# Performance work log

Measured on AMD Instinct MI355X. Metric: run time of the kernel, lower is better.

## Reference

```python
import itertools
import jax, jax.numpy as jnp
import numpy as np

GRID = 16384      # self.shape = (GRID,)
LAYERS = 8        # num_layers
SPAN = 2          # span = (2,)
K = 2 * SPAN + 1  # kernel size = 5 (ninputs)
NPOS = 2 ** K     # 32 possible boolean input combos
BATCH = 32
M = 4096          # x width; GRID % M == 0
STRIDE = GRID // M

# bitmask: all 2^K boolean input combinations, shape (NPOS, K)
_BITMASK = jnp.asarray(list(itertools.product(range(2), repeat=K)), dtype=jnp.float32)


def setup_inputs() -> dict:
    key = jax.random.key(0)
    k1, k2 = jax.random.split(key)
    x = jax.random.uniform(k1, (BATCH, M), dtype=jnp.float32)
    toggle_gates = jax.random.uniform(k2, (LAYERS, NPOS, GRID), dtype=jnp.float32)
    return {"x": x, "toggle_gates": toggle_gates}


def _convolve(state):
    # torch convolve(): offsets 0..K-1 via wrap-around roll, then spatial roll by
    # -SPAN to center the window -> neighbor n+i-SPAN (mod GRID) at kernel idx i.
    # jnp.roll(state, SPAN - i) gives out[:, n] = state[:, n + i - SPAN mod GRID].
    return jnp.stack([jnp.roll(state, SPAN - i, axis=1) for i in range(K)], axis=-1)  # (B, N, K)


def reference(x, toggle_gates):
    tw = jax.nn.sigmoid(toggle_gates)  # (L, NPOS, N)
    # embed(): scatter x evenly into the grid, rest is scratch (zeros)
    state = jnp.zeros((x.shape[0], GRID), dtype=x.dtype).at[:, ::STRIDE].set(x)

    def step(s, tw_layer):
        conv = _convolve(s)  # (B, N, K)
        # weight[c, b, n] = prod_i (1 - |bitmask[c, i] - conv[b, n, i]|)
        w = jnp.prod(1.0 - jnp.abs(_BITMASK[:, None, None, :] - conv[None]), axis=-1)  # (C, B, N)
        new = jnp.clip(jnp.einsum('cbn,cn->bn', w, tw_layer), 0.0, 1.0)
        return new, None

    state, _ = jax.lax.scan(step, state, tw)
    # forward returns state[slices] = state[:, ::STRIDE]
    return state[:, ::STRIDE]
```

## Files before the change

kernel.cpp:

```cpp
#include <hip/hip_runtime.h>

#define GRID_N 16384
#define NLAYERS 8
#define NPOS 32
#define BATCH 32
#define MW 4096
#define TILE 64
#define HALO 16
#define WBUF (TILE + 2 * HALO)

__global__ __launch_bounds__(256) void ASIC_44186623541335_kernel(
    const float* __restrict__ x,
    const float* __restrict__ tg,
    float* __restrict__ out)
{
    __shared__ float st[BATCH][WBUF];

    const int tid = threadIdx.x;
    const int tx  = tid & 63;
    const int ty  = tid >> 6;
    const int start = blockIdx.x * TILE;

    for (int f = tid; f < BATCH * WBUF; f += 256) {
        const int b = f / WBUF;
        const int j = f - b * WBUF;
        const int g = (start - HALO + j) & (GRID_N - 1);
        float v = 0.0f;
        if ((g & 3) == 0) v = x[b * MW + (g >> 2)];
        st[b][j] = v;
    }
    __syncthreads();

    float newv[2][8];

    for (int l = 0; l < NLAYERS; ++l) {
        const int h     = 2 * (NLAYERS - 1 - l);
        const int ncols = TILE + 2 * h;
        const int jbase = HALO - h;
        const float* twl = tg + (size_t)l * NPOS * GRID_N;

        #pragma unroll
        for (int p = 0; p < 2; ++p) {
            const int ci = tx + p * 64;
            if (ci < ncols) {
                const int j = jbase + ci;
                const int g = (start - h + ci) & (GRID_N - 1);

                float tw[32];
                #pragma unroll
                for (int c = 0; c < 32; ++c) {
                    const float v = twl[c * GRID_N + g];
                    tw[c] = __builtin_amdgcn_rcpf(1.0f + __expf(-v));
                }

                #pragma unroll
                for (int bb = 0; bb < 8; ++bb) {
                    const int b = ty * 8 + bb;
                    const float s0 = st[b][j - 2];
                    const float s1 = st[b][j - 1];
                    const float s2 = st[b][j];
                    const float s3 = st[b][j + 1];
                    const float s4 = st[b][j + 2];

                    float u[16];
                    #pragma unroll
                    for (int r = 0; r < 16; ++r)
                        u[r] = fmaf(s0, tw[16 + r] - tw[r], tw[r]);
                    #pragma unroll
                    for (int r = 0; r < 8; ++r)
                        u[r] = fmaf(s1, u[8 + r] - u[r], u[r]);
                    #pragma unroll
                    for (int r = 0; r < 4; ++r)
                        u[r] = fmaf(s2, u[4 + r] - u[r], u[r]);
                    #pragma unroll
                    for (int r = 0; r < 2; ++r)
                        u[r] = fmaf(s3, u[2 + r] - u[r], u[r]);
                    float res = fmaf(s4, u[1] - u[0], u[0]);
                    res = fminf(fmaxf(res, 0.0f), 1.0f);
                    newv[p][bb] = res;
                }
            }
        }
        __syncthreads();
        #pragma unroll
        for (int p = 0; p < 2; ++p) {
            const int ci = tx + p * 64;
            if (ci < ncols) {
                const int j = jbase + ci;
                #pragma unroll
                for (int bb = 0; bb < 8; ++bb)
                    st[ty * 8 + bb][j] = newv[p][bb];
            }
        }
        __syncthreads();
    }

    {
        const int g = start + tx;
        if ((g & 3) == 0) {
            const int m = g >> 2;
            #pragma unroll
            for (int bb = 0; bb < 8; ++bb) {
                const int b = ty * 8 + bb;
                out[b * MW + m] = st[b][HALO + tx];
            }
        }
    }
}

extern "C" void kernel_launch(void* const* d_in, const int* in_sizes, int n_in,
                              void* d_out, int out_size, void* d_ws, size_t ws_size,
                              hipStream_t stream) {
    const float* x  = (const float*)d_in[0];
    const float* tg = (const float*)d_in[1];
    float* out = (float*)d_out;
    ASIC_44186623541335_kernel<<<GRID_N / TILE, 256, 0, stream>>>(x, tg, out);
}
```

Before: 93.57 us.

## Halve tile, stage sigmoid gate weights in shared memory with layer-ahead prefetch

Shrinks the spatial tile from 64 to 32 columns, so the grid doubles to 512 blocks and each thread now covers one column instead of up to two. Gate weights for each layer are loaded cooperatively and coalesced, sigmoid is computed once per column into a padded shared-memory table, and the next layer's gates are prefetched into registers while the current layer computes. This replaces per-thread strided global loads and repeated sigmoid evaluation. The cost is more redundant halo work relative to the smaller tile, because the halo stays at 16 columns per side, plus extra shared memory.

```diff
diff --git a/kernel.cpp b/kernel.cpp
--- a/kernel.cpp
+++ b/kernel.cpp
@@ -5,9 +5,10 @@
 #define NPOS 32
 #define BATCH 32
 #define MW 4096
-#define TILE 64
+#define TILE 32
 #define HALO 16
-#define WBUF (TILE + 2 * HALO)
+#define WBUF 64
+#define TWPAD 33
 
 __global__ __launch_bounds__(256) void ASIC_44186623541335_kernel(
     const float* __restrict__ x,
@@ -15,95 +16,110 @@
     float* __restrict__ out)
 {
     __shared__ float st[BATCH][WBUF];
+    __shared__ float twl[WBUF][TWPAD];
 
     const int tid = threadIdx.x;
     const int tx  = tid & 63;
     const int ty  = tid >> 6;
     const int start = blockIdx.x * TILE;
+    const int gcol  = (start - HALO + tx) & (GRID_N - 1);
+
+    float pf[8];
+
+    #pragma unroll
+    for (int k = 0; k < 8; ++k) {
+        const int c = ty + 4 * k;
+        pf[k] = tg[(size_t)c * GRID_N + gcol];
+    }
 
     for (int f = tid; f < BATCH * WBUF; f += 256) {
-        const int b = f / WBUF;
-        const int j = f - b * WBUF;
+        const int b = f >> 6;
+        const int j = f & 63;
         const int g = (start - HALO + j) & (GRID_N - 1);
-        float v = 0.0f;
-        if ((g & 3) == 0) v = x[b * MW + (g >> 2)];
-        st[b][j] = v;
+        st[b][j] = ((g & 3) == 0) ? x[b * MW + (g >> 2)] : 0.0f;
+    }
+
+    #pragma unroll
+    for (int k = 0; k < 8; ++k) {
+        const int c = ty + 4 * k;
+        twl[tx][c] = __builtin_amdgcn_rcpf(1.0f + __expf(-pf[k]));
+    }
+    #pragma unroll
+    for (int k = 0; k < 8; ++k) {
+        const int c = ty + 4 * k;
+        pf[k] = tg[(size_t)NPOS * GRID_N + (size_t)c * GRID_N + gcol];
     }
     __syncthreads();
 
-    float newv[2][8];
-
+    float newv[8];
     for (int l = 0; l < NLAYERS; ++l) {
         const int h     = 2 * (NLAYERS - 1 - l);
         const int ncols = TILE + 2 * h;
-        const int jbase = HALO - h;
-        const float* twl = tg + (size_t)l * NPOS * GRID_N;
+        const int j     = (HALO - h) + tx;
+        const bool act  = tx < ncols;
 
-        #pragma unroll
-        for (int p = 0; p < 2; ++p) {
-            const int ci = tx + p * 64;
-            if (ci < ncols) {
-                const int j = jbase + ci;
-                const int g = (start - h + ci) & (GRID_N - 1);
+        if (act) {
+            float tw[32];
+            #pragma unroll
+            for (int c = 0; c < 32; ++c) tw[c] = twl[j][c];
 
-                float tw[32];
+            #pragma unroll
+            for (int bb = 0; bb < 8; ++bb) {
+                const int b = ty * 8 + bb;
+                const float s0 = st[b][j - 2];
+                const float s1 = st[b][j - 1];
+                const float s2 = st[b][j];
+                const float s3 = st[b][j + 1];
+                const float s4 = st[b][j + 2];
+
+                float u[16];
                 #pragma unroll
-                for (int c = 0; c < 32; ++c) {
-                    const float v = twl[c * GRID_N + g];
-                    tw[c] = __builtin_amdgcn_rcpf(1.0f + __expf(-v));
-                }
-
+                for (int r = 0; r < 16; ++r)
+                    u[r] = fmaf(s0, tw[16 + r] - tw[r], tw[r]);
                 #pragma unroll
-                for (int bb = 0; bb < 8; ++bb) {
-                    const int b = ty * 8 + bb;
-                    const float s0 = st[b][j - 2];
-                    const float s1 = st[b][j - 1];
-                    const float s2 = st[b][j];
-                    const float s3 = st[b][j + 1];
-                    const float s4 = st[b][j + 2];
-
-                    float u[16];
-                    #pragma unroll
-                    for (int r = 0; r < 16; ++r)
-                        u[r] = fmaf(s0, tw[16 + r] - tw[r], tw[r]);
-                    #pragma unroll
-                    for (int r = 0; r < 8; ++r)
-                        u[r] = fmaf(s1, u[8 + r] - u[r], u[r]);
-                    #pragma unroll
-                    for (int r = 0; r < 4; ++r)
-                        u[r] = fmaf(s2, u[4 + r] - u[r], u[r]);
-                    #pragma unroll
-                    for (int r = 0; r < 2; ++r)
-                        u[r] = fmaf(s3, u[2 + r] - u[r], u[r]);
-                    float res = fmaf(s4, u[1] - u[0], u[0]);
-                    res = fminf(fmaxf(res, 0.0f), 1.0f);
-                    newv[p][bb] = res;
-                }
+                for (int r = 0; r < 8; ++r)
+                    u[r] = fmaf(s1, u[8 + r] - u[r], u[r]);
+                #pragma unroll
+                for (int r = 0; r < 4; ++r)
+                    u[r] = fmaf(s2, u[4 + r] - u[r], u[r]);
+                #pragma unroll
+                for (int r = 0; r < 2; ++r)
+                    u[r] = fmaf(s3, u[2 + r] - u[r], u[r]);
+                float res = fmaf(s4, u[1] - u[0], u[0]);
+                newv[bb] = fminf(fmaxf(res, 0.0f), 1.0f);
             }
         }
         __syncthreads();
-        #pragma unroll
-        for (int p = 0; p < 2; ++p) {
-            const int ci = tx + p * 64;
-            if (ci < ncols) {
-                const int j = jbase + ci;
+
+        if (act) {
+            #pragma unroll
+            for (int bb = 0; bb < 8; ++bb)
+                st[ty * 8 + bb][j] = newv[bb];
+        }
+        if (l < NLAYERS - 1) {
+            #pragma unroll
+            for (int k = 0; k < 8; ++k) {
+                const int c = ty + 4 * k;
+                twl[tx][c] = __builtin_amdgcn_rcpf(1.0f + __expf(-pf[k]));
+            }
+            if (l + 2 < NLAYERS) {
+                const float* tn = tg + (size_t)(l + 2) * NPOS * GRID_N;
                 #pragma unroll
-                for (int bb = 0; bb < 8; ++bb)
-                    st[ty * 8 + bb][j] = newv[p][bb];
+                for (int k = 0; k < 8; ++k) {
+                    const int c = ty + 4 * k;
+                    pf[k] = tn[(size_t)c * GRID_N + gcol];
+                }
             }
         }
         __syncthreads();
     }
 
-    {
-        const int g = start + tx;
-        if ((g & 3) == 0) {
-            const int m = g >> 2;
-            #pragma unroll
-            for (int bb = 0; bb < 8; ++bb) {
-                const int b = ty * 8 + bb;
-                out[b * MW + m] = st[b][HALO + tx];
-            }
+    if (tx < TILE && (tx & 3) == 0) {
+        const int m = (start + tx) >> 2;
+        #pragma unroll
+        for (int bb = 0; bb < 8; ++bb) {
+            const int b = ty * 8 + bb;
+            out[b * MW + m] = st[b][HALO + tx];
         }
     }
 }
```

Result: faster. 81.79 us (-12.6%).
